# Kernel optimization log

Measured on AMD Instinct MI355X. Metric: run time of the kernel, lower is better.

## Reference

```python
import jax, jax.numpy as jnp
import numpy as np


def setup_inputs() -> dict:
    key = jax.random.key(0)
    k0, k1, k2, k3 = jax.random.split(key, 4)
    B, S, D, F, E = 2, 2048, 1024, 4096, 8
    scale = 0.02
    return {
        "x": jax.random.normal(k0, (B, S, D), jnp.float32),
        "gate_w": jax.random.normal(k1, (E, D), jnp.float32) * scale,
        "gate_b": jnp.zeros((E,), jnp.float32),
        "w1": jax.random.normal(k2, (E, D, F), jnp.float32) * scale,
        "b1": jnp.zeros((E, F), jnp.float32),
        "w2": jax.random.normal(k3, (E, F, D), jnp.float32) * scale,
        "b2": jnp.zeros((E, D), jnp.float32),
        "top_k": 2,
    }


def reference(x, gate_w, gate_b, w1, b1, w2, b2, top_k):
    B, S, D = x.shape
    E = gate_w.shape[0]
    xt = x.reshape(-1, D)                                   # [T, D]
    T = xt.shape[0]

    # Router: softmax over gate logits, then top-k and renormalize.
    gate_probs = jax.nn.softmax(xt @ gate_w.T + gate_b, axis=-1)   # [T, E]
    weights, selected = jax.lax.top_k(gate_probs, top_k)           # [T, k]
    weights = weights / jnp.sum(weights, axis=-1, keepdims=True)

    # Per-token combine weights over experts (zero where not selected),
    # equivalent to the per-expert gather/scatter loop in the original.
    combine = jnp.zeros((T, E), x.dtype).at[
        jnp.arange(T)[:, None], selected
    ].add(weights)                                                 # [T, E]

    # Expert MLPs (dense over experts, masked combine).
    h = jax.nn.silu(jnp.einsum("td,edf->etf", xt, w1) + b1[:, None, :])  # [E, T, F]
    expert_out = jnp.einsum("etf,efd->etd", h, w2) + b2[:, None, :]      # [E, T, D]
    out = jnp.einsum("etd,te->td", expert_out, combine)                  # [T, D]
    return out.reshape(B, S, D)
```

## Files before the change

### kernel.cpp

```cpp
#include <hip/hip_runtime.h>

#define T_TOK 4096
#define DIM   1024
#define FDIM  4096
#define NEXP  8

typedef __bf16 bf16x8 __attribute__((ext_vector_type(8)));
typedef float  f32x4  __attribute__((ext_vector_type(4)));

__device__ __forceinline__ void glds16(const void* g, void* l) {
    __builtin_amdgcn_global_load_lds(
        (const __attribute__((address_space(1))) void*)g,
        (__attribute__((address_space(3))) void*)l, 16, 0, 0);
}

__global__ __launch_bounds__(64)
void moe_router(const float* __restrict__ x,
                const float* __restrict__ gw,
                const float* __restrict__ gb,
                const int*   __restrict__ topk_p,
                int*   __restrict__ counts,
                int*   __restrict__ bucket,
                float* __restrict__ bweight) {
    const int t = blockIdx.x;
    const int lane = threadIdx.x;
    float part[NEXP];
#pragma unroll
    for (int e = 0; e < NEXP; ++e) part[e] = 0.f;
    const float* xrow = x + (size_t)t * DIM;
    for (int i = lane; i < DIM; i += 64) {
        float xv = xrow[i];
#pragma unroll
        for (int e = 0; e < NEXP; ++e) part[e] += xv * gw[e * DIM + i];
    }
#pragma unroll
    for (int off = 32; off > 0; off >>= 1) {
#pragma unroll
        for (int e = 0; e < NEXP; ++e) part[e] += __shfl_xor(part[e], off);
    }
    if (lane == 0) {
        int k = topk_p[0];
        if (k < 1) k = 1;
        if (k > NEXP) k = NEXP;
        float logit[NEXP];
        float mx = -1e30f;
#pragma unroll
        for (int e = 0; e < NEXP; ++e) {
            logit[e] = part[e] + gb[e];
            mx = fmaxf(mx, logit[e]);
        }
        float p[NEXP];
#pragma unroll
        for (int e = 0; e < NEXP; ++e) p[e] = __expf(logit[e] - mx);
        bool used[NEXP];
#pragma unroll
        for (int e = 0; e < NEXP; ++e) used[e] = false;
        int sel[NEXP]; float selp[NEXP]; float wsum = 0.f;
        for (int j = 0; j < k; ++j) {
            int best = 0; float bv = -1.f;
            for (int e = 0; e < NEXP; ++e)
                if (!used[e] && p[e] > bv) { bv = p[e]; best = e; }
            used[best] = true; sel[j] = best; selp[j] = bv; wsum += bv;
        }
        for (int j = 0; j < k; ++j) {
            int e = sel[j];
            int pos = atomicAdd(&counts[e], 1);
            bucket[e * T_TOK + pos]  = t;
            bweight[e * T_TOK + pos] = selp[j] / wsum;
        }
    }
}

__global__ __launch_bounds__(256)
void cvt_bf16(const float* __restrict__ in, __bf16* __restrict__ out) {
    size_t i = ((size_t)blockIdx.x * 256 + threadIdx.x) * 8;
    float4 v0 = *(const float4*)&in[i];
    float4 v1 = *(const float4*)&in[i + 4];
    bf16x8 t;
    t[0]=(__bf16)v0.x; t[1]=(__bf16)v0.y; t[2]=(__bf16)v0.z; t[3]=(__bf16)v0.w;
    t[4]=(__bf16)v1.x; t[5]=(__bf16)v1.y; t[6]=(__bf16)v1.z; t[7]=(__bf16)v1.w;
    *(bf16x8*)&out[i] = t;
}

__global__ __launch_bounds__(256)
void transpose_cvt(const float* __restrict__ in, __bf16* __restrict__ out,
                   int R, int C) {
    const size_t zo = (size_t)blockIdx.z * R * C;
    in += zo; out += zo;
    __shared__ float ts[64][65];
    const int c0 = blockIdx.x * 64, r0 = blockIdx.y * 64;
    const int t = threadIdx.x;
    const int rr = t >> 2, cc4 = (t & 3) * 16;
    const float* src = in + (size_t)(r0 + rr) * C + c0 + cc4;
#pragma unroll
    for (int i = 0; i < 4; ++i) {
        float4 v = *(const float4*)(src + i * 4);
        ts[rr][cc4 + i*4 + 0] = v.x; ts[rr][cc4 + i*4 + 1] = v.y;
        ts[rr][cc4 + i*4 + 2] = v.z; ts[rr][cc4 + i*4 + 3] = v.w;
    }
    __syncthreads();
    const int oc = rr, orc = cc4;
    bf16x8 o0, o1;
#pragma unroll
    for (int i = 0; i < 8; ++i) o0[i] = (__bf16)ts[orc + i][oc];
#pragma unroll
    for (int i = 0; i < 8; ++i) o1[i] = (__bf16)ts[orc + 8 + i][oc];
    __bf16* dst = out + (size_t)(c0 + oc) * R + r0 + orc;
    *(bf16x8*)dst = o0;
    *(bf16x8*)(dst + 8) = o1;
}

__global__ __launch_bounds__(64)
void build_work(const int* __restrict__ counts, int* __restrict__ hdr) {
    __shared__ int off1[NEXP + 1], off2[NEXP + 1];
    const int lane = threadIdx.x;
    if (lane == 0) {
        int a = 0, b = 0;
        for (int e = 0; e < NEXP; ++e) {
            off1[e] = a; off2[e] = b;
            a += (counts[e] + 127) >> 7;
            b += (counts[e] + 63) >> 6;
        }
        off1[NEXP] = a; off2[NEXP] = b;
        hdr[0] = a; hdr[1] = b;
    }
    __syncthreads();
    for (int e = 0; e < NEXP; ++e) {
        int n1 = off1[e + 1] - off1[e];
        for (int j = lane; j < n1; j += 64) hdr[8 + off1[e] + j] = (e << 16) | j;
        int n2 = off2[e + 1] - off2[e];
        for (int j = lane; j < n2; j += 64) hdr[264 + off2[e] + j] = (e << 16) | j;
    }
}

__global__ __launch_bounds__(256)
void moe_gemm1(const __bf16* __restrict__ xb,
               const __bf16* __restrict__ w1t,
               const float*  __restrict__ b1,
               const int*    __restrict__ counts,
               const int*    __restrict__ bucket,
               const int*    __restrict__ hdr,
               __bf16* __restrict__ H) {
    __shared__ __bf16 smem[8192];
    __shared__ int tok_s[128];
    const int tid = threadIdx.x;
    const int wave = tid >> 6, lane = tid & 63;
    const int wm = wave & 1, wn = wave >> 1;
    const int quad = lane >> 4, l15 = lane & 15;
    const int srow = tid >> 2, skc = (tid & 3) * 8;
    char* lA = (char*)smem + (size_t)wave * 1024;
    char* lB = (char*)smem + 8192 + (size_t)wave * 1024;

    const int n1 = hdr[0];
    const int total = n1 * (FDIM / 128);
    for (int u = blockIdx.x; u < total; u += gridDim.x) {
        const int entry = hdr[8 + (u % n1)];
        const int e = entry >> 16, tile = entry & 0xffff;
        const int nb = (u / n1) * 128;
        const int cnt = counts[e];
        if (tid < 128) {
            int r = tile * 128 + tid;
            if (r >= cnt) r = cnt - 1;
            tok_s[tid] = bucket[e * T_TOK + r];
        }
        __syncthreads();

        const __bf16* pa0 = xb + (size_t)tok_s[srow]      * DIM + skc;
        const __bf16* pa1 = xb + (size_t)tok_s[srow + 64] * DIM + skc;
        const __bf16* pb0 = w1t + ((size_t)e * FDIM + nb + srow) * DIM + skc;
        const __bf16* pb1 = pb0 + (size_t)64 * DIM;

        f32x4 acc[4][4];
#pragma unroll
        for (int i = 0; i < 4; ++i)
#pragma unroll
            for (int j = 0; j < 4; ++j) acc[i][j] = (f32x4){0.f,0.f,0.f,0.f};

        for (int k0 = 0; k0 < DIM; k0 += 32) {
            glds16(pa0 + k0, lA);
            glds16(pa1 + k0, lA + 4096);
            glds16(pb0 + k0, lB);
            glds16(pb1 + k0, lB + 4096);
            __syncthreads();
            bf16x8 af[4], bfr[4];
#pragma unroll
            for (int i = 0; i < 4; ++i)
                af[i] = *(const bf16x8*)&smem[(wm*64 + i*16 + l15)*32 + quad*8];
#pragma unroll
            for (int j = 0; j < 4; ++j)
                bfr[j] = *(const bf16x8*)&smem[4096 + (wn*64 + j*16 + l15)*32 + quad*8];
#pragma unroll
            for (int i = 0; i < 4; ++i)
#pragma unroll
                for (int j = 0; j < 4; ++j)
                    acc[i][j] = __builtin_amdgcn_mfma_f32_16x16x32_bf16(
                        af[i], bfr[j], acc[i][j], 0, 0, 0);
            __syncthreads();
        }

        __bf16* stg = smem + wave * 2048;
        const float* b1e = b1 + e * FDIM + nb + wn * 64;
#pragma unroll
        for (int i = 0; i < 4; ++i) {
#pragma unroll
            for (int j = 0; j < 4; ++j) {
                float bias = b1e[j * 16 + l15];
#pragma unroll
                for (int r = 0; r < 4; ++r) {
                    float v = acc[i][j][r] + bias;
                    float s = v / (1.f + __expf(-v));
                    stg[(quad*4 + r) * 68 + j*16 + l15] = (__bf16)s;
                }
            }
            __syncthreads();
            int rr = lane >> 2, coff = (lane & 3) * 16;
            int prow = tile * 128 + wm * 64 + i * 16 + rr;
            if (prow < cnt) {
                bf16x8 v0 = *(const bf16x8*)&stg[rr * 68 + coff];
                bf16x8 v1 = *(const bf16x8*)&stg[rr * 68 + coff + 8];
                __bf16* dst = H + (size_t)(e * T_TOK + prow) * FDIM
                              + nb + wn * 64 + coff;
                *(bf16x8*)dst = v0;
                *(bf16x8*)(dst + 8) = v1;
            }
            __syncthreads();
        }
    }
}

__global__ __launch_bounds__(256)
void moe_gemm2(const __bf16* __restrict__ H,
               const __bf16* __restrict__ w2t,
               const float*  __restrict__ b2,
               const int*    __restrict__ counts,
               const int*    __restrict__ bucket,
               const float*  __restrict__ bweight,
               const int*    __restrict__ hdr,
               float* __restrict__ out) {
    __shared__ __bf16 smem[6144];
    __shared__ int   tok_s[64];
    __shared__ float w_s[64];
    const int tid = threadIdx.x;
    const int wave = tid >> 6, lane = tid & 63;
    const int wm = wave & 1, wn = wave >> 1;
    const int quad = lane >> 4, l15 = lane & 15;
    const int srow = tid >> 2, skc = (tid & 3) * 8;
    char* lA = (char*)smem + (size_t)wave * 1024;
    char* lB = (char*)smem + 4096 + (size_t)wave * 1024;

    const int n2 = hdr[1];
    const int total = n2 * (DIM / 128);
    for (int u = blockIdx.x; u < total; u += gridDim.x) {
        const int entry = hdr[264 + (u % n2)];
        const int e = entry >> 16, tile = entry & 0xffff;
        const int nb = (u / n2) * 128;
        const int cnt = counts[e];
        if (tid < 64) {
            int r = tile * 64 + tid;
            int rc = r < cnt ? r : cnt - 1;
            tok_s[tid] = bucket[e * T_TOK + rc];
            w_s[tid]   = bweight[e * T_TOK + rc];
        }
        __syncthreads();

        const __bf16* pa  = H + (size_t)(e * T_TOK + tile * 64 + srow) * FDIM + skc;
        const __bf16* pb0 = w2t + ((size_t)e * DIM + nb + srow) * FDIM + skc;
        const __bf16* pb1 = pb0 + (size_t)64 * FDIM;

        f32x4 acc[2][4];
#pragma unroll
        for (int i = 0; i < 2; ++i)
#pragma unroll
            for (int j = 0; j < 4; ++j) acc[i][j] = (f32x4){0.f,0.f,0.f,0.f};

        for (int k0 = 0; k0 < FDIM; k0 += 32) {
            glds16(pa  + k0, lA);
            glds16(pb0 + k0, lB);
            glds16(pb1 + k0, lB + 4096);
            __syncthreads();
            bf16x8 af[2], bfr[4];
#pragma unroll
            for (int i = 0; i < 2; ++i)
                af[i] = *(const bf16x8*)&smem[(wm*32 + i*16 + l15)*32 + quad*8];
#pragma unroll
            for (int j = 0; j < 4; ++j)
                bfr[j] = *(const bf16x8*)&smem[2048 + (wn*64 + j*16 + l15)*32 + quad*8];
#pragma unroll
            for (int i = 0; i < 2; ++i)
#pragma unroll
                for (int j = 0; j < 4; ++j)
                    acc[i][j] = __builtin_amdgcn_mfma_f32_16x16x32_bf16(
                        af[i], bfr[j], acc[i][j], 0, 0, 0);
            __syncthreads();
        }

#pragma unroll
        for (int i = 0; i < 2; ++i)
#pragma unroll
            for (int j = 0; j < 4; ++j)
#pragma unroll
                for (int r = 0; r < 4; ++r) {
                    int m = wm*32 + i*16 + quad*4 + r;
                    int prow = tile * 64 + m;
                    if (prow < cnt) {
                        int dc = nb + wn*64 + j*16 + l15;
                        float v = acc[i][j][r] + b2[e * DIM + dc];
                        atomicAdd(&out[(size_t)tok_s[m] * DIM + dc], w_s[m] * v);
                    }
                }
        __syncthreads();
    }
}

extern "C" void kernel_launch(void* const* d_in, const int* in_sizes, int n_in,
                              void* d_out, int out_size, void* d_ws, size_t ws_size,
                              hipStream_t stream) {
    const float* x  = (const float*)d_in[0];
    const float* gw = (const float*)d_in[1];
    const float* gb = (const float*)d_in[2];
    const float* w1 = (const float*)d_in[3];
    const float* b1 = (const float*)d_in[4];
    const float* w2 = (const float*)d_in[5];
    const float* b2 = (const float*)d_in[6];
    const int* topk = (const int*)d_in[7];
    float* out = (float*)d_out;

    char* ws = (char*)d_ws;
    size_t off = 0;
    int* counts = (int*)(ws + off);    off += 256;
    int* bucket = (int*)(ws + off);    off += (size_t)NEXP * T_TOK * 4;
    float* bw   = (float*)(ws + off);  off += (size_t)NEXP * T_TOK * 4;
    int* hdr    = (int*)(ws + off);    off += 4096;
    off = (off + 255) & ~(size_t)255;
    __bf16* xb  = (__bf16*)(ws + off); off += (size_t)T_TOK * DIM * 2;
    __bf16* w1t = (__bf16*)(ws + off); off += (size_t)NEXP * DIM * FDIM * 2;
    __bf16* w2t = (__bf16*)(ws + off); off += (size_t)NEXP * FDIM * DIM * 2;
    __bf16* H   = (__bf16*)(ws + off);

    hipMemsetAsync(counts, 0, 256, stream);
    hipMemsetAsync(out, 0, (size_t)out_size * 4, stream);

    moe_router<<<T_TOK, 64, 0, stream>>>(x, gw, gb, topk, counts, bucket, bw);
    cvt_bf16<<<(T_TOK * DIM) / 2048, 256, 0, stream>>>(x, xb);
    transpose_cvt<<<dim3(FDIM/64, DIM/64, NEXP), 256, 0, stream>>>(w1, w1t, DIM, FDIM);
    transpose_cvt<<<dim3(DIM/64, FDIM/64, NEXP), 256, 0, stream>>>(w2, w2t, FDIM, DIM);
    build_work<<<1, 64, 0, stream>>>(counts, hdr);

    moe_gemm1<<<1024, 256, 0, stream>>>(xb, w1t, b1, counts, bucket, hdr, H);
    moe_gemm2<<<1024, 256, 0, stream>>>(H, w2t, b2, counts, bucket, bw, hdr, out);
}
```

Before: 861.7 us.

## Fuse bf16 cast into router, widen K step and enlarge gemm2 tiles

The x-to-bf16 conversion moves into the router kernel, which also vectorises its gate dot-product, so one launch and one read of x go away. Both expert GEMMs now load a 64-wide K slab per barrier pair with each wave loading only its own rows, halving synchronisation per K. gemm2 moves from 64x128 to 128x128 tiles sharing the gemm1 work list, which gives more reuse of the weights but fewer tiles and more registers. The gemm1 epilogue drops its per-row barriers and launch bounds now request 3 blocks per CU.

```diff
diff --git a/kernel.cpp b/kernel.cpp
--- a/kernel.cpp
+++ b/kernel.cpp
@@ -6,6 +6,7 @@
 #define NEXP  8
 
 typedef __bf16 bf16x8 __attribute__((ext_vector_type(8)));
+typedef __bf16 bf16x4 __attribute__((ext_vector_type(4)));
 typedef float  f32x4  __attribute__((ext_vector_type(4)));
 
 __device__ __forceinline__ void glds16(const void* g, void* l) {
@@ -21,17 +22,26 @@
                 const int*   __restrict__ topk_p,
                 int*   __restrict__ counts,
                 int*   __restrict__ bucket,
-                float* __restrict__ bweight) {
+                float* __restrict__ bweight,
+                __bf16* __restrict__ xb) {
     const int t = blockIdx.x;
     const int lane = threadIdx.x;
     float part[NEXP];
 #pragma unroll
     for (int e = 0; e < NEXP; ++e) part[e] = 0.f;
     const float* xrow = x + (size_t)t * DIM;
-    for (int i = lane; i < DIM; i += 64) {
-        float xv = xrow[i];
-#pragma unroll
-        for (int e = 0; e < NEXP; ++e) part[e] += xv * gw[e * DIM + i];
+    __bf16* xbrow = xb + (size_t)t * DIM;
+#pragma unroll
+    for (int r = 0; r < 4; ++r) {
+        int c = r * 256 + lane * 4;
+        float4 v = *(const float4*)&xrow[c];
+        bf16x4 o; o[0]=(__bf16)v.x; o[1]=(__bf16)v.y; o[2]=(__bf16)v.z; o[3]=(__bf16)v.w;
+        *(bf16x4*)&xbrow[c] = o;
+#pragma unroll
+        for (int e = 0; e < NEXP; ++e) {
+            float4 g = *(const float4*)&gw[e * DIM + c];
+            part[e] += v.x*g.x + v.y*g.y + v.z*g.z + v.w*g.w;
+        }
     }
 #pragma unroll
     for (int off = 32; off > 0; off >>= 1) {
@@ -42,16 +52,15 @@
         int k = topk_p[0];
         if (k < 1) k = 1;
         if (k > NEXP) k = NEXP;
-        float logit[NEXP];
+        float p[NEXP];
         float mx = -1e30f;
 #pragma unroll
         for (int e = 0; e < NEXP; ++e) {
-            logit[e] = part[e] + gb[e];
-            mx = fmaxf(mx, logit[e]);
-        }
-        float p[NEXP];
-#pragma unroll
-        for (int e = 0; e < NEXP; ++e) p[e] = __expf(logit[e] - mx);
+            p[e] = part[e] + gb[e];
+            mx = fmaxf(mx, p[e]);
+        }
+#pragma unroll
+        for (int e = 0; e < NEXP; ++e) p[e] = __expf(p[e] - mx);
         bool used[NEXP];
 #pragma unroll
         for (int e = 0; e < NEXP; ++e) used[e] = false;
@@ -69,17 +78,6 @@
             bweight[e * T_TOK + pos] = selp[j] / wsum;
         }
     }
-}
-
-__global__ __launch_bounds__(256)
-void cvt_bf16(const float* __restrict__ in, __bf16* __restrict__ out) {
-    size_t i = ((size_t)blockIdx.x * 256 + threadIdx.x) * 8;
-    float4 v0 = *(const float4*)&in[i];
-    float4 v1 = *(const float4*)&in[i + 4];
-    bf16x8 t;
-    t[0]=(__bf16)v0.x; t[1]=(__bf16)v0.y; t[2]=(__bf16)v0.z; t[3]=(__bf16)v0.w;
-    t[4]=(__bf16)v1.x; t[5]=(__bf16)v1.y; t[6]=(__bf16)v1.z; t[7]=(__bf16)v1.w;
-    *(bf16x8*)&out[i] = t;
 }
 
 __global__ __launch_bounds__(256)
@@ -112,28 +110,26 @@
 
 __global__ __launch_bounds__(64)
 void build_work(const int* __restrict__ counts, int* __restrict__ hdr) {
-    __shared__ int off1[NEXP + 1], off2[NEXP + 1];
+    __shared__ int off1[NEXP + 1];
     const int lane = threadIdx.x;
     if (lane == 0) {
-        int a = 0, b = 0;
+        int a = 0;
         for (int e = 0; e < NEXP; ++e) {
-            off1[e] = a; off2[e] = b;
+            off1[e] = a;
             a += (counts[e] + 127) >> 7;
-            b += (counts[e] + 63) >> 6;
-        }
-        off1[NEXP] = a; off2[NEXP] = b;
-        hdr[0] = a; hdr[1] = b;
+        }
+        off1[NEXP] = a;
+        hdr[0] = a;
     }
     __syncthreads();
     for (int e = 0; e < NEXP; ++e) {
         int n1 = off1[e + 1] - off1[e];
         for (int j = lane; j < n1; j += 64) hdr[8 + off1[e] + j] = (e << 16) | j;
-        int n2 = off2[e + 1] - off2[e];
-        for (int j = lane; j < n2; j += 64) hdr[264 + off2[e] + j] = (e << 16) | j;
-    }
-}
-
-__global__ __launch_bounds__(256)
+    }
+}
+
+
+__global__ __launch_bounds__(256, 3)
 void moe_gemm1(const __bf16* __restrict__ xb,
                const __bf16* __restrict__ w1t,
                const float*  __restrict__ b1,
@@ -141,15 +137,19 @@
                const int*    __restrict__ bucket,
                const int*    __restrict__ hdr,
                __bf16* __restrict__ H) {
-    __shared__ __bf16 smem[8192];
+    __shared__ __bf16 smem[16384];
     __shared__ int tok_s[128];
     const int tid = threadIdx.x;
     const int wave = tid >> 6, lane = tid & 63;
     const int wm = wave & 1, wn = wave >> 1;
     const int quad = lane >> 4, l15 = lane & 15;
-    const int srow = tid >> 2, skc = (tid & 3) * 8;
-    char* lA = (char*)smem + (size_t)wave * 1024;
-    char* lB = (char*)smem + 8192 + (size_t)wave * 1024;
+    const int lrow = lane >> 2;
+    const int lk8  = (lane & 3) * 8;
+    char* sb = (char*)smem;
+    char* dA0 = sb + wave * 2048;
+    char* dA1 = sb + 8192 + wave * 2048;
+    char* dB0 = sb + 16384 + wave * 2048;
+    char* dB1 = sb + 24576 + wave * 2048;
 
     const int n1 = hdr[0];
     const int total = n1 * (FDIM / 128);
@@ -165,10 +165,11 @@
         }
         __syncthreads();
 
-        const __bf16* pa0 = xb + (size_t)tok_s[srow]      * DIM + skc;
-        const __bf16* pa1 = xb + (size_t)tok_s[srow + 64] * DIM + skc;
-        const __bf16* pb0 = w1t + ((size_t)e * FDIM + nb + srow) * DIM + skc;
-        const __bf16* pb1 = pb0 + (size_t)64 * DIM;
+        const int ar0 = wave * 32 + lrow;
+        const __bf16* pA0 = xb + (size_t)tok_s[ar0]      * DIM + lk8;
+        const __bf16* pA1 = xb + (size_t)tok_s[ar0 + 16] * DIM + lk8;
+        const __bf16* pB0 = w1t + ((size_t)e * FDIM + nb + wave * 32 + lrow) * DIM + lk8;
+        const __bf16* pB1 = pB0 + (size_t)16 * DIM;
 
         f32x4 acc[4][4];
 #pragma unroll
@@ -176,29 +177,36 @@
 #pragma unroll
             for (int j = 0; j < 4; ++j) acc[i][j] = (f32x4){0.f,0.f,0.f,0.f};
 
-        for (int k0 = 0; k0 < DIM; k0 += 32) {
-            glds16(pa0 + k0, lA);
-            glds16(pa1 + k0, lA + 4096);
-            glds16(pb0 + k0, lB);
-            glds16(pb1 + k0, lB + 4096);
+        for (int k0 = 0; k0 < DIM; k0 += 64) {
+            glds16(pA0 + k0,      dA0);
+            glds16(pA0 + k0 + 32, dA1);
+            glds16(pA1 + k0,      dA0 + 1024);
+            glds16(pA1 + k0 + 32, dA1 + 1024);
+            glds16(pB0 + k0,      dB0);
+            glds16(pB0 + k0 + 32, dB1);
+            glds16(pB1 + k0,      dB0 + 1024);
+            glds16(pB1 + k0 + 32, dB1 + 1024);
             __syncthreads();
-            bf16x8 af[4], bfr[4];
-#pragma unroll
-            for (int i = 0; i < 4; ++i)
-                af[i] = *(const bf16x8*)&smem[(wm*64 + i*16 + l15)*32 + quad*8];
-#pragma unroll
-            for (int j = 0; j < 4; ++j)
-                bfr[j] = *(const bf16x8*)&smem[4096 + (wn*64 + j*16 + l15)*32 + quad*8];
-#pragma unroll
-            for (int i = 0; i < 4; ++i)
+#pragma unroll
+            for (int kk = 0; kk < 2; ++kk) {
+                bf16x8 af[4], bfr[4];
+#pragma unroll
+                for (int i = 0; i < 4; ++i)
+                    af[i] = *(const bf16x8*)&smem[kk*4096 + (wm*64 + i*16 + l15)*32 + quad*8];
 #pragma unroll
                 for (int j = 0; j < 4; ++j)
-                    acc[i][j] = __builtin_amdgcn_mfma_f32_16x16x32_bf16(
-                        af[i], bfr[j], acc[i][j], 0, 0, 0);
+                    bfr[j] = *(const bf16x8*)&smem[8192 + kk*4096 + (wn*64 + j*16 + l15)*32 + quad*8];
+#pragma unroll
+                for (int i = 0; i < 4; ++i)
+#pragma unroll
+                    for (int j = 0; j < 4; ++j)
+                        acc[i][j] = __builtin_amdgcn_mfma_f32_16x16x32_bf16(
+                            af[i], bfr[j], acc[i][j], 0, 0, 0);
+            }
             __syncthreads();
         }
 
-        __bf16* stg = smem + wave * 2048;
+        __bf16* stg = (__bf16*)(sb + wave * 2304);
         const float* b1e = b1 + e * FDIM + nb + wn * 64;
 #pragma unroll
         for (int i = 0; i < 4; ++i) {
@@ -209,26 +217,24 @@
                 for (int r = 0; r < 4; ++r) {
                     float v = acc[i][j][r] + bias;
                     float s = v / (1.f + __expf(-v));
-                    stg[(quad*4 + r) * 68 + j*16 + l15] = (__bf16)s;
+                    stg[(quad*4 + r) * 72 + j*16 + l15] = (__bf16)s;
                 }
             }
-            __syncthreads();
-            int rr = lane >> 2, coff = (lane & 3) * 16;
-            int prow = tile * 128 + wm * 64 + i * 16 + rr;
+            int prow = tile * 128 + wm * 64 + i * 16 + lrow;
             if (prow < cnt) {
-                bf16x8 v0 = *(const bf16x8*)&stg[rr * 68 + coff];
-                bf16x8 v1 = *(const bf16x8*)&stg[rr * 68 + coff + 8];
+                bf16x8 v0 = *(const bf16x8*)&stg[lrow * 72 + (lane & 3) * 16];
+                bf16x8 v1 = *(const bf16x8*)&stg[lrow * 72 + (lane & 3) * 16 + 8];
                 __bf16* dst = H + (size_t)(e * T_TOK + prow) * FDIM
-                              + nb + wn * 64 + coff;
+                              + nb + wn * 64 + (lane & 3) * 16;
                 *(bf16x8*)dst = v0;
                 *(bf16x8*)(dst + 8) = v1;
             }
-            __syncthreads();
-        }
-    }
-}
-
-__global__ __launch_bounds__(256)
+        }
+        __syncthreads();
+    }
+}
+
+__global__ __launch_bounds__(256, 3)
 void moe_gemm2(const __bf16* __restrict__ H,
                const __bf16* __restrict__ w2t,
                const float*  __restrict__ b2,
@@ -237,71 +243,84 @@
                const float*  __restrict__ bweight,
                const int*    __restrict__ hdr,
                float* __restrict__ out) {
-    __shared__ __bf16 smem[6144];
-    __shared__ int   tok_s[64];
-    __shared__ float w_s[64];
+    __shared__ __bf16 smem[16384];
+    __shared__ int   tok_s[128];
+    __shared__ float w_s[128];
     const int tid = threadIdx.x;
     const int wave = tid >> 6, lane = tid & 63;
     const int wm = wave & 1, wn = wave >> 1;
     const int quad = lane >> 4, l15 = lane & 15;
-    const int srow = tid >> 2, skc = (tid & 3) * 8;
-    char* lA = (char*)smem + (size_t)wave * 1024;
-    char* lB = (char*)smem + 4096 + (size_t)wave * 1024;
-
-    const int n2 = hdr[1];
-    const int total = n2 * (DIM / 128);
+    const int lrow = lane >> 2;
+    const int lk8  = (lane & 3) * 8;
+    char* sb = (char*)smem;
+    char* dA0 = sb + wave * 2048;
+    char* dA1 = sb + 8192 + wave * 2048;
+    char* dB0 = sb + 16384 + wave * 2048;
+    char* dB1 = sb + 24576 + wave * 2048;
+
+    const int n1 = hdr[0];
+    const int total = n1 * (DIM / 128);
     for (int u = blockIdx.x; u < total; u += gridDim.x) {
-        const int entry = hdr[264 + (u % n2)];
+        const int entry = hdr[8 + (u % n1)];
         const int e = entry >> 16, tile = entry & 0xffff;
-        const int nb = (u / n2) * 128;
+        const int nb = (u / n1) * 128;
         const int cnt = counts[e];
-        if (tid < 64) {
-            int r = tile * 64 + tid;
+        if (tid < 128) {
+            int r  = tile * 128 + tid;
             int rc = r < cnt ? r : cnt - 1;
             tok_s[tid] = bucket[e * T_TOK + rc];
             w_s[tid]   = bweight[e * T_TOK + rc];
         }
         __syncthreads();
 
-        const __bf16* pa  = H + (size_t)(e * T_TOK + tile * 64 + srow) * FDIM + skc;
-        const __bf16* pb0 = w2t + ((size_t)e * DIM + nb + srow) * FDIM + skc;
-        const __bf16* pb1 = pb0 + (size_t)64 * FDIM;
-
-        f32x4 acc[2][4];
-#pragma unroll
-        for (int i = 0; i < 2; ++i)
+        const __bf16* pA0 = H + (size_t)(e * T_TOK + tile * 128 + wave * 32 + lrow) * FDIM + lk8;
+        const __bf16* pA1 = pA0 + (size_t)16 * FDIM;
+        const __bf16* pB0 = w2t + ((size_t)e * DIM + nb + wave * 32 + lrow) * FDIM + lk8;
+        const __bf16* pB1 = pB0 + (size_t)16 * FDIM;
+
+        f32x4 acc[4][4];
+#pragma unroll
+        for (int i = 0; i < 4; ++i)
 #pragma unroll
             for (int j = 0; j < 4; ++j) acc[i][j] = (f32x4){0.f,0.f,0.f,0.f};
 
-        for (int k0 = 0; k0 < FDIM; k0 += 32) {
-            glds16(pa  + k0, lA);
-            glds16(pb0 + k0, lB);
-            glds16(pb1 + k0, lB + 4096);
+        for (int k0 = 0; k0 < FDIM; k0 += 64) {
+            glds16(pA0 + k0,      dA0);
+            glds16(pA0 + k0 + 32, dA1);
+            glds16(pA1 + k0,      dA0 + 1024);
+            glds16(pA1 + k0 + 32, dA1 + 1024);
+            glds16(pB0 + k0,      dB0);
+            glds16(pB0 + k0 + 32, dB1);
+            glds16(pB1 + k0,      dB0 + 1024);
+            glds16(pB1 + k0 + 32, dB1 + 1024);
             __syncthreads();
-            bf16x8 af[2], bfr[4];
-#pragma unroll
-            for (int i = 0; i < 2; ++i)
-                af[i] = *(const bf16x8*)&smem[(wm*32 + i*16 + l15)*32 + quad*8];
+#pragma unroll
+            for (int kk = 0; kk < 2; ++kk) {
+                bf16x8 af[4], bfr[4];
+#pragma unroll
+                for (int i = 0; i < 4; ++i)
+                    af[i] = *(const bf16x8*)&smem[kk*4096 + (wm*64 + i*16 + l15)*32 + quad*8];
+#pragma unroll
+                for (int j = 0; j < 4; ++j)
+                    bfr[j] = *(const bf16x8*)&smem[8192 + kk*4096 + (wn*64 + j*16 + l15)*32 + quad*8];
+#pragma unroll
+                for (int i = 0; i < 4; ++i)
+#pragma unroll
+                    for (int j = 0; j < 4; ++j)
+                        acc[i][j] = __builtin_amdgcn_mfma_f32_16x16x32_bf16(
+                            af[i], bfr[j], acc[i][j], 0, 0, 0);
+            }
+            __syncthreads();
+        }
+
+#pragma unroll
+        for (int i = 0; i < 4; ++i)
 #pragma unroll
             for (int j = 0; j < 4; ++j)
-                bfr[j] = *(const bf16x8*)&smem[2048 + (wn*64 + j*16 + l15)*32 + quad*8];
-#pragma unroll
-            for (int i = 0; i < 2; ++i)
-#pragma unroll
-                for (int j = 0; j < 4; ++j)
-                    acc[i][j] = __builtin_amdgcn_mfma_f32_16x16x32_bf16(
-                        af[i], bfr[j], acc[i][j], 0, 0, 0);
-            __syncthreads();
-        }
-
-#pragma unroll
-        for (int i = 0; i < 2; ++i)
-#pragma unroll
-            for (int j = 0; j < 4; ++j)
 #pragma unroll
                 for (int r = 0; r < 4; ++r) {
-                    int m = wm*32 + i*16 + quad*4 + r;
-                    int prow = tile * 64 + m;
+                    int m = wm*64 + i*16 + quad*4 + r;
+                    int prow = tile * 128 + m;
                     if (prow < cnt) {
                         int dc = nb + wn*64 + j*16 + l15;
                         float v = acc[i][j][r] + b2[e * DIM + dc];
@@ -340,12 +359,11 @@
     hipMemsetAsync(counts, 0, 256, stream);
     hipMemsetAsync(out, 0, (size_t)out_size * 4, stream);
 
-    moe_router<<<T_TOK, 64, 0, stream>>>(x, gw, gb, topk, counts, bucket, bw);
-    cvt_bf16<<<(T_TOK * DIM) / 2048, 256, 0, stream>>>(x, xb);
+    moe_router<<<T_TOK, 64, 0, stream>>>(x, gw, gb, topk, counts, bucket, bw, xb);
     transpose_cvt<<<dim3(FDIM/64, DIM/64, NEXP), 256, 0, stream>>>(w1, w1t, DIM, FDIM);
     transpose_cvt<<<dim3(DIM/64, FDIM/64, NEXP), 256, 0, stream>>>(w2, w2t, FDIM, DIM);
     build_work<<<1, 64, 0, stream>>>(counts, hdr);
 
     moe_gemm1<<<1024, 256, 0, stream>>>(xb, w1t, b1, counts, bucket, hdr, H);
-    moe_gemm2<<<1024, 256, 0, stream>>>(H, w2t, b2, counts, bucket, bw, hdr, out);
-}
+    moe_gemm2<<<512, 256, 0, stream>>>(H, w2t, b2, counts, bucket, bw, hdr, out);
+}
```

Result: faster. 824.8 us (-4.3%).
